# Kernel tuning notes

Measured on AMD Instinct MI355X. Metric: run time of the kernel, lower is better.

## Reference

```python
import jax, jax.numpy as jnp
import numpy as np
from jax import lax

BN_EPS = 1e-5
LN_EPS = 1e-5
EPS = 1e-6


def _bn(x, g, b, m, v):
    inv = g / jnp.sqrt(v + BN_EPS)
    return (x - m[None, :, None, None]) * inv[None, :, None, None] + b[None, :, None, None]


def _conv1x1(x, w, b=None):
    y = jnp.einsum('bchw,oc->bohw', x, w)
    if b is not None:
        y = y + b[None, :, None, None]
    return y


def _conv2d(x, w, pad_h, pad_w):
    return lax.conv_general_dilated(x, w, (1, 1), [(pad_h, pad_h), (pad_w, pad_w)],
                                    dimension_numbers=('NCHW', 'OIHW', 'NCHW'))


def _haar_dwt(x):
    # Haar analysis, stride-2: pure 2x2 add/sub arithmetic (H, W assumed even).
    B, C, H, W = x.shape
    xb = x.reshape(B, C, H // 2, 2, W // 2, 2)
    x00 = xb[:, :, :, 0, :, 0]; x01 = xb[:, :, :, 0, :, 1]
    x10 = xb[:, :, :, 1, :, 0]; x11 = xb[:, :, :, 1, :, 1]
    LL = 0.5 * (x00 + x01 + x10 + x11)
    LH = 0.5 * (-x00 + x01 - x10 + x11)
    HL = 0.5 * (-x00 - x01 + x10 + x11)
    HH = 0.5 * (x00 - x01 - x10 + x11)
    return LH, HL, HH, LL


def _haar_idwt(LH, HL, HH, LL):
    # Matches conv_transpose2d(stride=2) with the same Haar kernels.
    x00 = 0.5 * (LL - LH - HL + HH); x01 = 0.5 * (LL + LH - HL - HH)
    x10 = 0.5 * (LL - LH + HL - HH); x11 = 0.5 * (LL + LH + HL + HH)
    B, C, h, w = LL.shape
    top = jnp.stack([x00, x01], axis=-1)  # (B,C,h,w,2)
    bot = jnp.stack([x10, x11], axis=-1)
    y = jnp.stack([top, bot], axis=3)     # (B,C,h,2,w,2)
    return y.reshape(B, C, 2 * h, 2 * w)


def _soft_threshold(x, thr):
    return jnp.sign(x) * jax.nn.relu(jnp.abs(x) - thr)


def _forward(x, red_w, red_bias, red_bn_g, red_bn_b, red_bn_m, red_bn_v,
             gct_fc1_w, gct_fc1_b, gct_ln_g, gct_ln_b, gct_fc2_w, gct_fc2_b,
             rel_h_w, rel_h_b, rel_h_bn_g, rel_h_bn_b, rel_h_bn_m, rel_h_bn_v,
             rel_v_w, rel_v_b, rel_v_bn_g, rel_v_bn_b, rel_v_bn_m, rel_v_bn_v,
             rel_fus_w, rel_fus_b, hw_theta, hw_fuse_w, hw_fc_w, hw_fc_b,
             sf_w, sf_b, sf_bn_g, sf_bn_b, sf_bn_m, sf_bn_v, fin_w, fin_b):
    B, C, H, W = x.shape
    split = C // 2  # alpha = 0.5
    identity = x[:, :split]
    gate = x[:, split:]
    r = jax.nn.relu(_bn(_conv1x1(gate, red_w, red_bias), red_bn_g, red_bn_b, red_bn_m, red_bn_v))
    # --- GCT stream: GAP -> Linear -> LayerNorm -> ReLU -> Linear -> sigmoid gate ---
    ctx = r.mean(axis=(2, 3))                      # (B,Cr)
    h1 = ctx @ gct_fc1_w.T + gct_fc1_b
    mu = h1.mean(-1, keepdims=True)
    var = ((h1 - mu) ** 2).mean(-1, keepdims=True)
    h1 = (h1 - mu) / jnp.sqrt(var + LN_EPS) * gct_ln_g + gct_ln_b
    w_gct = jax.nn.sigmoid(jax.nn.relu(h1) @ gct_fc2_w.T + gct_fc2_b)
    gct_out = r * w_gct[:, :, None, None]
    # --- Rel stream: anisotropic pool -> conv/BN/ReLU -> bilinear(size-1 axis == broadcast) ---
    hf = _conv2d(r.mean(axis=2, keepdims=True), rel_h_w, 0, 1) + rel_h_b[None, :, None, None]
    hf = jax.nn.relu(_bn(hf, rel_h_bn_g, rel_h_bn_b, rel_h_bn_m, rel_h_bn_v))
    hf = jnp.broadcast_to(hf, (B, hf.shape[1], H, W))
    vf = _conv2d(r.mean(axis=3, keepdims=True), rel_v_w, 1, 0) + rel_v_b[None, :, None, None]
    vf = jax.nn.relu(_bn(vf, rel_v_bn_g, rel_v_bn_b, rel_v_bn_m, rel_v_bn_v))
    vf = jnp.broadcast_to(vf, (B, vf.shape[1], H, W))
    rel_w_map = jax.nn.sigmoid(_conv1x1(jnp.concatenate([hf, vf], axis=1), rel_fus_w, rel_fus_b))
    rel_out = r * rel_w_map
    # --- HWFE / wavelet attention ---
    LH, HL, HH, LL = _haar_dwt(r)
    t = jax.nn.sigmoid(hw_theta)                   # (3,Cr,1,1)
    m_LH = jnp.abs(LH).mean(axis=(2, 3), keepdims=True) + EPS
    m_HL = jnp.abs(HL).mean(axis=(2, 3), keepdims=True) + EPS
    m_HH = jnp.abs(HH).mean(axis=(2, 3), keepdims=True) + EPS
    LH_h = _soft_threshold(LH, t[0][None] * m_LH)
    HL_h = _soft_threshold(HL, t[1][None] * m_HL)
    HH_h = _soft_threshold(HH, t[2][None] * m_HH)
    fused = _conv1x1(jnp.concatenate([LH_h, HL_h, HH_h], axis=1), hw_fuse_w)
    X_re = _haar_idwt(LH_h, HL_h, fused, LL)       # note: fused sits in HH slot, as in source
    gap = X_re.mean(axis=(2, 3)) @ hw_fc_w.T + hw_fc_b
    attn = jax.nn.softmax(gap, axis=1)
    hwfe_out = r * attn[:, :, None, None]
    # --- stream fusion + gating ---
    interaction = gct_out * rel_out + hwfe_out
    gate_weight = jax.nn.sigmoid(_bn(_conv1x1(interaction, sf_w, sf_b), sf_bn_g, sf_bn_b, sf_bn_m, sf_bn_v))
    out = jnp.concatenate([identity, gate * gate_weight], axis=1)
    return _conv1x1(out, fin_w, fin_b)


def setup_inputs() -> dict:
    key = jax.random.key(0)
    ks = jax.random.split(key, 20)
    B, C, H, W = 16, 512, 64, 64
    Cg = C // 2           # gate channels = 256
    Cr = 16               # max(4, 256 // 16)
    Ch = Cr // 2          # 8
    Hd = max(1, Cr // 4)  # 4
    f = lambda k, s: jax.random.normal(k, s, jnp.float32) * 0.05
    return dict(
        x=jax.random.normal(ks[0], (B, C, H, W), jnp.float32),
        red_w=f(ks[1], (Cr, Cg)), red_bias=f(ks[2], (Cr,)),
        red_bn_g=jnp.ones((Cr,)), red_bn_b=jnp.zeros((Cr,)),
        red_bn_m=jnp.zeros((Cr,)), red_bn_v=jnp.ones((Cr,)),
        gct_fc1_w=f(ks[3], (Hd, Cr)), gct_fc1_b=f(ks[4], (Hd,)),
        gct_ln_g=jnp.ones((Hd,)), gct_ln_b=jnp.zeros((Hd,)),
        gct_fc2_w=f(ks[5], (Cr, Hd)), gct_fc2_b=f(ks[6], (Cr,)),
        rel_h_w=f(ks[7], (Ch, Cr, 1, 3)), rel_h_b=f(ks[8], (Ch,)),
        rel_h_bn_g=jnp.ones((Ch,)), rel_h_bn_b=jnp.zeros((Ch,)),
        rel_h_bn_m=jnp.zeros((Ch,)), rel_h_bn_v=jnp.ones((Ch,)),
        rel_v_w=f(ks[9], (Ch, Cr, 3, 1)), rel_v_b=f(ks[10], (Ch,)),
        rel_v_bn_g=jnp.ones((Ch,)), rel_v_bn_b=jnp.zeros((Ch,)),
        rel_v_bn_m=jnp.zeros((Ch,)), rel_v_bn_v=jnp.ones((Ch,)),
        rel_fus_w=f(ks[11], (Cr, 2 * Ch)), rel_fus_b=f(ks[12], (Cr,)),
        hw_theta=f(ks[13], (3, Cr, 1, 1)), hw_fuse_w=f(ks[14], (Cr, 3 * Cr)),
        hw_fc_w=f(ks[15], (Cr, Cr)), hw_fc_b=f(ks[16], (Cr,)),
        sf_w=f(ks[17], (Cg, Cr)), sf_b=f(ks[18], (Cg,)),
        sf_bn_g=jnp.ones((Cg,)), sf_bn_b=jnp.zeros((Cg,)),
        sf_bn_m=jnp.zeros((Cg,)), sf_bn_v=jnp.ones((Cg,)),
        fin_w=f(ks[19], (C, C)), fin_b=jnp.zeros((C,)),
    )


def reference(x, red_w, red_bias, red_bn_g, red_bn_b, red_bn_m, red_bn_v,
              gct_fc1_w, gct_fc1_b, gct_ln_g, gct_ln_b, gct_fc2_w, gct_fc2_b,
              rel_h_w, rel_h_b, rel_h_bn_g, rel_h_bn_b, rel_h_bn_m, rel_h_bn_v,
              rel_v_w, rel_v_b, rel_v_bn_g, rel_v_bn_b, rel_v_bn_m, rel_v_bn_v,
              rel_fus_w, rel_fus_b, hw_theta, hw_fuse_w, hw_fc_w, hw_fc_b,
              sf_w, sf_b, sf_bn_g, sf_bn_b, sf_bn_m, sf_bn_v, fin_w, fin_b):
    return _forward(x, red_w, red_bias, red_bn_g, red_bn_b, red_bn_m, red_bn_v,
                    gct_fc1_w, gct_fc1_b, gct_ln_g, gct_ln_b, gct_fc2_w, gct_fc2_b,
                    rel_h_w, rel_h_b, rel_h_bn_g, rel_h_bn_b, rel_h_bn_m, rel_h_bn_v,
                    rel_v_w, rel_v_b, rel_v_bn_g, rel_v_bn_b, rel_v_bn_m, rel_v_bn_v,
                    rel_fus_w, rel_fus_b, hw_theta, hw_fuse_w, hw_fc_w, hw_fc_b,
                    sf_w, sf_b, sf_bn_g, sf_bn_b, sf_bn_m, sf_bn_v, fin_w, fin_b)
```

## Files before the change

### kernel.cpp

```cpp
#include <hip/hip_runtime.h>
#include <cstdint>

typedef uint16_t u16;
typedef uint32_t u32;
typedef uint64_t u64;
typedef __attribute__((ext_vector_type(4))) float f32x4;
typedef __attribute__((ext_vector_type(8))) short bf16x8;

__device__ __forceinline__ u16 f2bf(float f) {
  union { float f; u32 i; } u; u.f = f;
  u32 r = u.i + 0x7FFFu + ((u.i >> 16) & 1u);
  return (u16)(r >> 16);
}
__device__ __forceinline__ float sigm(float x) { return 1.f / (1.f + __expf(-x)); }

__global__ __launch_bounds__(256) void k0_pack(
    const float* __restrict__ fw, u16* __restrict__ fwb)
{
  int i = blockIdx.x * 256 + threadIdx.x;
  f32x4 v = ((const f32x4*)fw)[i];
  u64 p = (u64)f2bf(v[0]) | ((u64)f2bf(v[1]) << 16) |
          ((u64)f2bf(v[2]) << 32) | ((u64)f2bf(v[3]) << 48);
  ((u64*)fwb)[i] = p;
}

__global__ __launch_bounds__(256) void k1_reduce(
    const float* __restrict__ x, const float* __restrict__ rw, const float* __restrict__ rb,
    const float* __restrict__ bg, const float* __restrict__ bb, const float* __restrict__ bm,
    const float* __restrict__ bv, float* __restrict__ r)
{
  __shared__ __align__(16) float wl[256][16];
  __shared__ float bl[16];
  __shared__ float sl[16];
  int t = threadIdx.x;
  if (t < 16) {
    float s = bg[t] * rsqrtf(bv[t] + 1e-5f);
    sl[t] = s;
    bl[t] = (rb[t] - bm[t]) * s + bb[t];
  }
  __syncthreads();
  for (int i = 0; i < 16; ++i) {
    int flat = i * 256 + t;
    int co = flat >> 8, c = flat & 255;
    wl[c][co] = rw[co * 256 + c] * sl[co];
  }
  __syncthreads();
  int p = blockIdx.x * 256 + t;
  int b = p >> 12, pp = p & 4095;
  const float* gsrc = x + ((size_t)(b * 512 + 256)) * 4096 + pp;
  float acc[16];
#pragma unroll
  for (int co = 0; co < 16; ++co) acc[co] = bl[co];
#pragma unroll 4
  for (int c = 0; c < 256; ++c) {
    float g = gsrc[(size_t)c * 4096];
    const f32x4* wr = (const f32x4*)(&wl[c][0]);
    f32x4 a0 = wr[0], a1 = wr[1], a2 = wr[2], a3 = wr[3];
    acc[0]  += g * a0[0]; acc[1]  += g * a0[1]; acc[2]  += g * a0[2]; acc[3]  += g * a0[3];
    acc[4]  += g * a1[0]; acc[5]  += g * a1[1]; acc[6]  += g * a1[2]; acc[7]  += g * a1[3];
    acc[8]  += g * a2[0]; acc[9]  += g * a2[1]; acc[10] += g * a2[2]; acc[11] += g * a2[3];
    acc[12] += g * a3[0]; acc[13] += g * a3[1]; acc[14] += g * a3[2]; acc[15] += g * a3[3];
  }
  float* rd = r + ((size_t)b * 16) * 4096 + pp;
#pragma unroll
  for (int co = 0; co < 16; ++co) rd[(size_t)co * 4096] = fmaxf(acc[co], 0.f);
}

__global__ __launch_bounds__(256) void k2_means(
    const float* __restrict__ r, float* __restrict__ cm, float* __restrict__ rm,
    float* __restrict__ ctx)
{
  __shared__ __align__(16) float tile[64][68];
  int bc = blockIdx.x, t = threadIdx.x;
  const float* src = r + (size_t)bc * 4096;
#pragma unroll
  for (int i = 0; i < 4; ++i) {
    int off = (i * 256 + t) * 4;
    int row = off >> 6, col = off & 63;
    f32x4 v = *(const f32x4*)(src + off);
    *(f32x4*)&tile[row][col] = v;
  }
  __syncthreads();
  int wv = t >> 6, lane = t & 63;
  if (wv == 0) {
    float s = 0.f;
    for (int h = 0; h < 64; ++h) s += tile[h][lane];
    cm[bc * 64 + lane] = s * (1.f / 64.f);
    float tot = s;
#pragma unroll
    for (int m = 32; m; m >>= 1) tot += __shfl_xor(tot, m, 64);
    if (lane == 0) ctx[bc] = tot * (1.f / 4096.f);
  } else if (wv == 1) {
    float s = 0.f;
    for (int w0 = 0; w0 < 64; ++w0) s += tile[lane][(w0 + lane) & 63];
    rm[bc * 64 + lane] = s * (1.f / 64.f);
  }
}

__global__ __launch_bounds__(256) void k3a_gct(
    const float* __restrict__ ctx,
    const float* f1w, const float* f1b, const float* lng, const float* lnb,
    const float* f2w, const float* f2b, const float* fcw, const float* fcb,
    float* __restrict__ wgct, float* __restrict__ attn)
{
  __shared__ float cl[256];
  __shared__ float gl[256];
  int t = threadIdx.x;
  cl[t] = ctx[t];
  __syncthreads();
  int b = t >> 4, c = t & 15;
  const float* cb = &cl[b * 16];
  float a[4];
#pragma unroll
  for (int j = 0; j < 4; ++j) {
    float s = f1b[j];
    for (int i = 0; i < 16; ++i) s += cb[i] * f1w[j * 16 + i];
    a[j] = s;
  }
  float mu = 0.25f * (a[0] + a[1] + a[2] + a[3]);
  float var = 0.f;
#pragma unroll
  for (int j = 0; j < 4; ++j) { float d = a[j] - mu; var += d * d; }
  var *= 0.25f;
  float inv = rsqrtf(var + 1e-5f);
#pragma unroll
  for (int j = 0; j < 4; ++j)
    a[j] = fmaxf((a[j] - mu) * inv * lng[j] + lnb[j], 0.f);
  float s2 = f2b[c];
#pragma unroll
  for (int j = 0; j < 4; ++j) s2 += a[j] * f2w[c * 4 + j];
  wgct[t] = sigm(s2);
  float g = fcb[c];
  for (int i = 0; i < 16; ++i) g += cb[i] * fcw[c * 16 + i];
  gl[t] = g;
  __syncthreads();
  const float* gb = &gl[b * 16];
  float mx = -1e30f;
  for (int i = 0; i < 16; ++i) mx = fmaxf(mx, gb[i]);
  float den = 0.f;
  for (int i = 0; i < 16; ++i) den += __expf(gb[i] - mx);
  attn[t] = __expf(g - mx) / den;
}

__global__ __launch_bounds__(64) void k3b_rel(
    const float* __restrict__ cm, const float* __restrict__ rm,
    const float* hw, const float* hb, const float* hbg, const float* hbb, const float* hbm, const float* hbv,
    const float* vw, const float* vb_, const float* vbg, const float* vbb, const float* vbm, const float* vbv,
    const float* fw, const float* fb, float* __restrict__ hfc, float* __restrict__ vfc)
{
  __shared__ float cml[16][64], rml[16][64];
  int b = blockIdx.x, t = threadIdx.x;
  for (int i = 0; i < 16; ++i) {
    cml[i][t] = cm[(b * 16 + i) * 64 + t];
    rml[i][t] = rm[(b * 16 + i) * 64 + t];
  }
  __syncthreads();
  float hf[8], vf[8];
  for (int o = 0; o < 8; ++o) {
    float sh = 0.f, sv = 0.f;
    for (int ci = 0; ci < 16; ++ci) {
#pragma unroll
      for (int kk = 0; kk < 3; ++kk) {
        int q = t + kk - 1;
        bool ok = (q >= 0 && q < 64);
        int qi = ok ? q : 0;
        float xh = ok ? cml[ci][qi] : 0.f;
        float xv = ok ? rml[ci][qi] : 0.f;
        sh += hw[(o * 16 + ci) * 3 + kk] * xh;
        sv += vw[(o * 16 + ci) * 3 + kk] * xv;
      }
    }
    float s1 = hbg[o] * rsqrtf(hbv[o] + 1e-5f);
    hf[o] = fmaxf((sh + hb[o] - hbm[o]) * s1 + hbb[o], 0.f);
    float s2 = vbg[o] * rsqrtf(vbv[o] + 1e-5f);
    vf[o] = fmaxf((sv + vb_[o] - vbm[o]) * s2 + vbb[o], 0.f);
  }
  for (int o = 0; o < 16; ++o) {
    float sh = fb[o], sv = 0.f;
#pragma unroll
    for (int c = 0; c < 8; ++c) {
      sh += fw[o * 16 + c] * hf[c];
      sv += fw[o * 16 + 8 + c] * vf[c];
    }
    hfc[(b * 16 + o) * 64 + t] = sh;
    vfc[(b * 16 + o) * 64 + t] = sv;
  }
}

__global__ __launch_bounds__(512, 4) void k45_v2(
    const float* __restrict__ x, const float* __restrict__ r,
    const float* __restrict__ wgct, const float* __restrict__ attn,
    const float* __restrict__ hfc, const float* __restrict__ vfc,
    const float* __restrict__ sfw, const float* __restrict__ sfb,
    const float* __restrict__ sg, const float* __restrict__ sb_,
    const float* __restrict__ sbm, const float* __restrict__ sbv,
    const u16* __restrict__ fwb, const float* __restrict__ fb,
    float* __restrict__ out)
{
  __shared__ __align__(16) u16 A[64 * 528];
  __shared__ float wgs[16], ats[16], vfhs[16];
  char* Ab = (char*)A;

  int bid = blockIdx.x;
  int b = bid >> 6, h = bid & 63;
  int t = threadIdx.x;

  if (t < 16) {
    wgs[t]  = wgct[b * 16 + t];
    ats[t]  = attn[b * 16 + t];
    vfhs[t] = vfc[(b * 16 + t) * 64 + h];
  }
  if (t < 256) {
    int o = t;
    float s = sg[o] * rsqrtf(sbv[o] + 1e-5f);
    float* wrow = (float*)(Ab + (o & 63) * 1056 + 512 + (o >> 6) * 64);
#pragma unroll
    for (int k2 = 0; k2 < 16; ++k2) wrow[k2] = sfw[o * 16 + k2] * s;
    *(float*)(Ab + (o & 63) * 1056 + 768 + (o >> 6) * 4) =
        (sfb[o] - sbm[o]) * s + sb_[o];
  }
  __syncthreads();

#pragma unroll
  for (int i = 0; i < 2; ++i) {
    int idx = i * 512 + t;
    int k = idx >> 6, w = idx & 63;
    float rv = r[((size_t)(b * 16 + k)) * 4096 + h * 64 + w];
    float rel = sigm(hfc[(b * 16 + k) * 64 + w] + vfhs[k]);
    *(float*)(Ab + w * 1056 + 784 + k * 4) =
        rv * rv * wgs[k] * rel + rv * ats[k];
  }
  __syncthreads();

  {
    int w = t & 63, og = t >> 6;
    float iv[16];
#pragma unroll
    for (int k2 = 0; k2 < 16; ++k2)
      iv[k2] = *(const float*)(Ab + w * 1056 + 784 + k2 * 4);
    const float* gsrc = x + ((size_t)(b * 512 + 256)) * 4096 + h * 64 + w;
    for (int j = 0; j < 32; ++j) {
      int o = og * 32 + j;
      const f32x4* wr = (const f32x4*)(Ab + (o & 63) * 1056 + 512 + (o >> 6) * 64);
      f32x4 w0 = wr[0], w1 = wr[1], w2 = wr[2], w3 = wr[3];
      float dot = *(const float*)(Ab + (o & 63) * 1056 + 768 + (o >> 6) * 4);
      dot += iv[0]  * w0[0] + iv[1]  * w0[1] + iv[2]  * w0[2] + iv[3]  * w0[3];
      dot += iv[4]  * w1[0] + iv[5]  * w1[1] + iv[6]  * w1[2] + iv[7]  * w1[3];
      dot += iv[8]  * w2[0] + iv[9]  * w2[1] + iv[10] * w2[2] + iv[11] * w2[3];
      dot += iv[12] * w3[0] + iv[13] * w3[1] + iv[14] * w3[2] + iv[15] * w3[3];
      float gwv = sigm(dot);
      float gv = gsrc[(size_t)o * 4096];
      A[w * 528 + o] = f2bf(gv * gwv);
    }
  }
  __syncthreads();

#pragma unroll
  for (int i = 0; i < 8; ++i) {
    int flat = i * 512 + t;
    int c = flat >> 4, q = flat & 15;
    f32x4 v = *(const f32x4*)(x + ((size_t)(b * 512 + c)) * 4096 + h * 64 + q * 4);
#pragma unroll
    for (int j = 0; j < 4; ++j) A[(q * 4 + j) * 528 + 256 + c] = f2bf(v[j]);
  }
  __syncthreads();

  int lane = t & 63, wv = t >> 6;
  int fr = lane & 15, quad = lane >> 4;
  int n0w = wv * 64;
  f32x4 acc[4][4];
#pragma unroll
  for (int j = 0; j < 4; ++j) {
    float bvv = fb[n0w + j * 16 + fr];
    f32x4 b4 = {bvv, bvv, bvv, bvv};
#pragma unroll
    for (int i = 0; i < 4; ++i) acc[i][j] = b4;
  }
  const u16* Bp = fwb + (size_t)(n0w + fr) * 512 + quad * 8;
  for (int kb = 0; kb < 16; ++kb) {
    int c0 = kb * 32 + quad * 8;
    int kbb = kb ^ 8;
    bf16x8 af[4], bfr[4];
#pragma unroll
    for (int i = 0; i < 4; ++i)
      af[i] = *(const bf16x8*)(A + (i * 16 + fr) * 528 + c0);
#pragma unroll
    for (int j = 0; j < 4; ++j)
      bfr[j] = *(const bf16x8*)(Bp + (size_t)(j * 16) * 512 + kbb * 32);
#pragma unroll
    for (int j = 0; j < 4; ++j)
#pragma unroll
      for (int i = 0; i < 4; ++i)
        acc[i][j] = __builtin_amdgcn_mfma_f32_16x16x32_bf16(af[i], bfr[j], acc[i][j], 0, 0, 0);
  }

  float* ob = out + ((size_t)(b * 512 + n0w + fr)) * 4096 + h * 64 + quad * 4;
#pragma unroll
  for (int j = 0; j < 4; ++j)
#pragma unroll
    for (int i = 0; i < 4; ++i)
      *(f32x4*)(ob + (size_t)(j * 16) * 4096 + i * 16) = acc[i][j];
}

extern "C" void kernel_launch(void* const* d_in, const int* in_sizes, int n_in,
                              void* d_out, int out_size, void* d_ws, size_t ws_size,
                              hipStream_t stream) {
  const float* x      = (const float*)d_in[0];
  const float* red_w  = (const float*)d_in[1];
  const float* red_b  = (const float*)d_in[2];
  const float* rbg    = (const float*)d_in[3];
  const float* rbb    = (const float*)d_in[4];
  const float* rbm    = (const float*)d_in[5];
  const float* rbv    = (const float*)d_in[6];
  const float* f1w    = (const float*)d_in[7];
  const float* f1b    = (const float*)d_in[8];
  const float* lng    = (const float*)d_in[9];
  const float* lnb    = (const float*)d_in[10];
  const float* f2w    = (const float*)d_in[11];
  const float* f2b    = (const float*)d_in[12];
  const float* rhw    = (const float*)d_in[13];
  const float* rhb    = (const float*)d_in[14];
  const float* rhbg   = (const float*)d_in[15];
  const float* rhbb   = (const float*)d_in[16];
  const float* rhbm   = (const float*)d_in[17];
  const float* rhbv   = (const float*)d_in[18];
  const float* rvw    = (const float*)d_in[19];
  const float* rvb    = (const float*)d_in[20];
  const float* rvbg   = (const float*)d_in[21];
  const float* rvbb   = (const float*)d_in[22];
  const float* rvbm   = (const float*)d_in[23];
  const float* rvbv   = (const float*)d_in[24];
  const float* fusw   = (const float*)d_in[25];
  const float* fusb   = (const float*)d_in[26];
  const float* fcw    = (const float*)d_in[29];
  const float* fcb    = (const float*)d_in[30];
  const float* sfw    = (const float*)d_in[31];
  const float* sfb    = (const float*)d_in[32];
  const float* sbg    = (const float*)d_in[33];
  const float* sbb    = (const float*)d_in[34];
  const float* sbm    = (const float*)d_in[35];
  const float* sbv    = (const float*)d_in[36];
  const float* finw   = (const float*)d_in[37];
  const float* finb   = (const float*)d_in[38];
  float* out = (float*)d_out;

  char* ws = (char*)d_ws;
  size_t off = 0;
  float* r   = (float*)(ws + off); off += (size_t)16 * 16 * 4096 * 4;
  u16*   fwb = (u16*)(ws + off);   off += (size_t)512 * 512 * 2;
  float* cm  = (float*)(ws + off); off += 65536;
  float* rm  = (float*)(ws + off); off += 65536;
  float* ctx = (float*)(ws + off); off += 1024;
  float* wg  = (float*)(ws + off); off += 1024;
  float* at  = (float*)(ws + off); off += 1024;
  float* hfc = (float*)(ws + off); off += 65536;
  float* vfc = (float*)(ws + off); off += 65536;

  k0_pack<<<256, 256, 0, stream>>>(finw, fwb);
  k1_reduce<<<256, 256, 0, stream>>>(x, red_w, red_b, rbg, rbb, rbm, rbv, r);
  k2_means<<<256, 256, 0, stream>>>(r, cm, rm, ctx);
  k3a_gct<<<1, 256, 0, stream>>>(ctx, f1w, f1b, lng, lnb, f2w, f2b, fcw, fcb, wg, at);
  k3b_rel<<<16, 64, 0, stream>>>(cm, rm, rhw, rhb, rhbg, rhbb, rhbm, rhbv,
                                 rvw, rvb, rvbg, rvbb, rvbm, rvbv, fusw, fusb, hfc, vfc);
  k45_v2<<<1024, 512, 0, stream>>>(x, r, wg, at, hfc, vfc,
                                   sfw, sfb, sbg, sbb, sbm, sbv, fwb, finb, out);
}
```

Baseline: 440.4 us.

## Merge small prologue kernels into one launch and vectorize LDS staging in main kernel

The weight-pack, GCT and relation kernels become one launch, with the block index choosing the branch, so two launches and their serialization gaps go away. The main kernel removes one barrier, shrinks the LDS row stride, and writes the gated tile as 8-wide bf16 vectors instead of scalar u16 stores. The identity-channel transpose now uses ds_bpermute lane shuffles so each lane packs four bf16 values into a single 64-bit LDS store. The reduce loop unroll also goes from 4 to 8. These changes add shuffle instructions and rely on the new stride giving acceptable LDS bank behaviour.

```diff
diff --git a/kernel.cpp b/kernel.cpp
--- a/kernel.cpp
+++ b/kernel.cpp
@@ -13,16 +13,6 @@
   return (u16)(r >> 16);
 }
 __device__ __forceinline__ float sigm(float x) { return 1.f / (1.f + __expf(-x)); }
-
-__global__ __launch_bounds__(256) void k0_pack(
-    const float* __restrict__ fw, u16* __restrict__ fwb)
-{
-  int i = blockIdx.x * 256 + threadIdx.x;
-  f32x4 v = ((const f32x4*)fw)[i];
-  u64 p = (u64)f2bf(v[0]) | ((u64)f2bf(v[1]) << 16) |
-          ((u64)f2bf(v[2]) << 32) | ((u64)f2bf(v[3]) << 48);
-  ((u64*)fwb)[i] = p;
-}
 
 __global__ __launch_bounds__(256) void k1_reduce(
     const float* __restrict__ x, const float* __restrict__ rw, const float* __restrict__ rb,
@@ -51,7 +41,7 @@
   float acc[16];
 #pragma unroll
   for (int co = 0; co < 16; ++co) acc[co] = bl[co];
-#pragma unroll 4
+#pragma unroll 8
   for (int c = 0; c < 256; ++c) {
     float g = gsrc[(size_t)c * 4096];
     const f32x4* wr = (const f32x4*)(&wl[c][0]);
@@ -97,97 +87,108 @@
   }
 }
 
-__global__ __launch_bounds__(256) void k3a_gct(
+__global__ __launch_bounds__(256) void k3x(
+    const float* __restrict__ finw, u16* __restrict__ fwb,
     const float* __restrict__ ctx,
     const float* f1w, const float* f1b, const float* lng, const float* lnb,
     const float* f2w, const float* f2b, const float* fcw, const float* fcb,
-    float* __restrict__ wgct, float* __restrict__ attn)
-{
-  __shared__ float cl[256];
-  __shared__ float gl[256];
-  int t = threadIdx.x;
-  cl[t] = ctx[t];
-  __syncthreads();
-  int b = t >> 4, c = t & 15;
-  const float* cb = &cl[b * 16];
-  float a[4];
-#pragma unroll
-  for (int j = 0; j < 4; ++j) {
-    float s = f1b[j];
-    for (int i = 0; i < 16; ++i) s += cb[i] * f1w[j * 16 + i];
-    a[j] = s;
-  }
-  float mu = 0.25f * (a[0] + a[1] + a[2] + a[3]);
-  float var = 0.f;
-#pragma unroll
-  for (int j = 0; j < 4; ++j) { float d = a[j] - mu; var += d * d; }
-  var *= 0.25f;
-  float inv = rsqrtf(var + 1e-5f);
-#pragma unroll
-  for (int j = 0; j < 4; ++j)
-    a[j] = fmaxf((a[j] - mu) * inv * lng[j] + lnb[j], 0.f);
-  float s2 = f2b[c];
-#pragma unroll
-  for (int j = 0; j < 4; ++j) s2 += a[j] * f2w[c * 4 + j];
-  wgct[t] = sigm(s2);
-  float g = fcb[c];
-  for (int i = 0; i < 16; ++i) g += cb[i] * fcw[c * 16 + i];
-  gl[t] = g;
-  __syncthreads();
-  const float* gb = &gl[b * 16];
-  float mx = -1e30f;
-  for (int i = 0; i < 16; ++i) mx = fmaxf(mx, gb[i]);
-  float den = 0.f;
-  for (int i = 0; i < 16; ++i) den += __expf(gb[i] - mx);
-  attn[t] = __expf(g - mx) / den;
-}
-
-__global__ __launch_bounds__(64) void k3b_rel(
+    float* __restrict__ wgct, float* __restrict__ attn,
     const float* __restrict__ cm, const float* __restrict__ rm,
     const float* hw, const float* hb, const float* hbg, const float* hbb, const float* hbm, const float* hbv,
     const float* vw, const float* vb_, const float* vbg, const float* vbb, const float* vbm, const float* vbv,
     const float* fw, const float* fb, float* __restrict__ hfc, float* __restrict__ vfc)
 {
-  __shared__ float cml[16][64], rml[16][64];
-  int b = blockIdx.x, t = threadIdx.x;
-  for (int i = 0; i < 16; ++i) {
-    cml[i][t] = cm[(b * 16 + i) * 64 + t];
-    rml[i][t] = rm[(b * 16 + i) * 64 + t];
-  }
-  __syncthreads();
-  float hf[8], vf[8];
-  for (int o = 0; o < 8; ++o) {
-    float sh = 0.f, sv = 0.f;
-    for (int ci = 0; ci < 16; ++ci) {
-#pragma unroll
-      for (int kk = 0; kk < 3; ++kk) {
-        int q = t + kk - 1;
-        bool ok = (q >= 0 && q < 64);
-        int qi = ok ? q : 0;
-        float xh = ok ? cml[ci][qi] : 0.f;
-        float xv = ok ? rml[ci][qi] : 0.f;
-        sh += hw[(o * 16 + ci) * 3 + kk] * xh;
-        sv += vw[(o * 16 + ci) * 3 + kk] * xv;
+  int bid = blockIdx.x, t = threadIdx.x;
+  if (bid < 256) {
+    int i = bid * 256 + t;
+    f32x4 v = ((const f32x4*)finw)[i];
+    u64 p = (u64)f2bf(v[0]) | ((u64)f2bf(v[1]) << 16) |
+            ((u64)f2bf(v[2]) << 32) | ((u64)f2bf(v[3]) << 48);
+    ((u64*)fwb)[i] = p;
+  } else if (bid == 256) {
+    __shared__ float cl[256];
+    __shared__ float gl[256];
+    cl[t] = ctx[t];
+    __syncthreads();
+    int b = t >> 4, c = t & 15;
+    const float* cb = &cl[b * 16];
+    float a[4];
+#pragma unroll
+    for (int j = 0; j < 4; ++j) {
+      float s = f1b[j];
+      for (int i = 0; i < 16; ++i) s += cb[i] * f1w[j * 16 + i];
+      a[j] = s;
+    }
+    float mu = 0.25f * (a[0] + a[1] + a[2] + a[3]);
+    float var = 0.f;
+#pragma unroll
+    for (int j = 0; j < 4; ++j) { float d = a[j] - mu; var += d * d; }
+    var *= 0.25f;
+    float inv = rsqrtf(var + 1e-5f);
+#pragma unroll
+    for (int j = 0; j < 4; ++j)
+      a[j] = fmaxf((a[j] - mu) * inv * lng[j] + lnb[j], 0.f);
+    float s2 = f2b[c];
+#pragma unroll
+    for (int j = 0; j < 4; ++j) s2 += a[j] * f2w[c * 4 + j];
+    wgct[t] = sigm(s2);
+    float g = fcb[c];
+    for (int i = 0; i < 16; ++i) g += cb[i] * fcw[c * 16 + i];
+    gl[t] = g;
+    __syncthreads();
+    const float* gb = &gl[b * 16];
+    float mx = -1e30f;
+    for (int i = 0; i < 16; ++i) mx = fmaxf(mx, gb[i]);
+    float den = 0.f;
+    for (int i = 0; i < 16; ++i) den += __expf(gb[i] - mx);
+    attn[t] = __expf(g - mx) / den;
+  } else {
+    __shared__ float cml[16][64], rml[16][64];
+    int b = bid - 257;
+#pragma unroll
+    for (int i = 0; i < 4; ++i) {
+      int idx = i * 256 + t;
+      int row = idx >> 6, col = idx & 63;
+      cml[row][col] = cm[(b * 16 + row) * 64 + col];
+      rml[row][col] = rm[(b * 16 + row) * 64 + col];
+    }
+    __syncthreads();
+    if (t < 64) {
+      float hf[8], vf[8];
+      for (int o = 0; o < 8; ++o) {
+        float sh = 0.f, sv = 0.f;
+        for (int ci = 0; ci < 16; ++ci) {
+#pragma unroll
+          for (int kk = 0; kk < 3; ++kk) {
+            int q = t + kk - 1;
+            bool ok = (q >= 0 && q < 64);
+            int qi = ok ? q : 0;
+            float xh = ok ? cml[ci][qi] : 0.f;
+            float xv = ok ? rml[ci][qi] : 0.f;
+            sh += hw[(o * 16 + ci) * 3 + kk] * xh;
+            sv += vw[(o * 16 + ci) * 3 + kk] * xv;
+          }
+        }
+        float s1 = hbg[o] * rsqrtf(hbv[o] + 1e-5f);
+        hf[o] = fmaxf((sh + hb[o] - hbm[o]) * s1 + hbb[o], 0.f);
+        float s2 = vbg[o] * rsqrtf(vbv[o] + 1e-5f);
+        vf[o] = fmaxf((sv + vb_[o] - vbm[o]) * s2 + vbb[o], 0.f);
       }
-    }
-    float s1 = hbg[o] * rsqrtf(hbv[o] + 1e-5f);
-    hf[o] = fmaxf((sh + hb[o] - hbm[o]) * s1 + hbb[o], 0.f);
-    float s2 = vbg[o] * rsqrtf(vbv[o] + 1e-5f);
-    vf[o] = fmaxf((sv + vb_[o] - vbm[o]) * s2 + vbb[o], 0.f);
-  }
-  for (int o = 0; o < 16; ++o) {
-    float sh = fb[o], sv = 0.f;
-#pragma unroll
-    for (int c = 0; c < 8; ++c) {
-      sh += fw[o * 16 + c] * hf[c];
-      sv += fw[o * 16 + 8 + c] * vf[c];
-    }
-    hfc[(b * 16 + o) * 64 + t] = sh;
-    vfc[(b * 16 + o) * 64 + t] = sv;
-  }
-}
-
-__global__ __launch_bounds__(512, 4) void k45_v2(
+      for (int o = 0; o < 16; ++o) {
+        float sh = fb[o], sv = 0.f;
+#pragma unroll
+        for (int c = 0; c < 8; ++c) {
+          sh += fw[o * 16 + c] * hf[c];
+          sv += fw[o * 16 + 8 + c] * vf[c];
+        }
+        hfc[(b * 16 + o) * 64 + t] = sh;
+        vfc[(b * 16 + o) * 64 + t] = sv;
+      }
+    }
+  }
+}
+
+__global__ __launch_bounds__(512, 4) void k45_v3(
     const float* __restrict__ x, const float* __restrict__ r,
     const float* __restrict__ wgct, const float* __restrict__ attn,
     const float* __restrict__ hfc, const float* __restrict__ vfc,
@@ -197,75 +198,91 @@
     const u16* __restrict__ fwb, const float* __restrict__ fb,
     float* __restrict__ out)
 {
-  __shared__ __align__(16) u16 A[64 * 528];
-  __shared__ float wgs[16], ats[16], vfhs[16];
+  __shared__ __align__(16) u16 A[64 * 520];
   char* Ab = (char*)A;
 
   int bid = blockIdx.x;
   int b = bid >> 6, h = bid & 63;
   int t = threadIdx.x;
-
-  if (t < 16) {
-    wgs[t]  = wgct[b * 16 + t];
-    ats[t]  = attn[b * 16 + t];
-    vfhs[t] = vfc[(b * 16 + t) * 64 + h];
-  }
+  int lane = t & 63, wv = t >> 6;
+
   if (t < 256) {
     int o = t;
     float s = sg[o] * rsqrtf(sbv[o] + 1e-5f);
-    float* wrow = (float*)(Ab + (o & 63) * 1056 + 512 + (o >> 6) * 64);
-#pragma unroll
-    for (int k2 = 0; k2 < 16; ++k2) wrow[k2] = sfw[o * 16 + k2] * s;
-    *(float*)(Ab + (o & 63) * 1056 + 768 + (o >> 6) * 4) =
+    const f32x4* sw = (const f32x4*)(sfw + o * 16);
+    f32x4 w0 = sw[0] * s, w1 = sw[1] * s, w2 = sw[2] * s, w3 = sw[3] * s;
+    f32x4* wrow = (f32x4*)(Ab + (o & 63) * 1040 + 512 + (o >> 6) * 64);
+    wrow[0] = w0; wrow[1] = w1; wrow[2] = w2; wrow[3] = w3;
+    *(float*)(Ab + (o & 63) * 1040 + 768 + (o >> 6) * 4) =
         (sfb[o] - sbm[o]) * s + sb_[o];
   }
-  __syncthreads();
-
 #pragma unroll
   for (int i = 0; i < 2; ++i) {
     int idx = i * 512 + t;
     int k = idx >> 6, w = idx & 63;
     float rv = r[((size_t)(b * 16 + k)) * 4096 + h * 64 + w];
-    float rel = sigm(hfc[(b * 16 + k) * 64 + w] + vfhs[k]);
-    *(float*)(Ab + w * 1056 + 784 + k * 4) =
-        rv * rv * wgs[k] * rel + rv * ats[k];
+    float rel = sigm(hfc[(b * 16 + k) * 64 + w] + vfc[(b * 16 + k) * 64 + h]);
+    *(float*)(Ab + w * 1040 + 784 + k * 4) =
+        rv * rv * wgct[b * 16 + k] * rel + rv * attn[b * 16 + k];
   }
   __syncthreads();
 
   {
     int w = t & 63, og = t >> 6;
-    float iv[16];
-#pragma unroll
-    for (int k2 = 0; k2 < 16; ++k2)
-      iv[k2] = *(const float*)(Ab + w * 1056 + 784 + k2 * 4);
+    const char* irow = Ab + w * 1040 + 784;
+    f32x4 iv0 = *(const f32x4*)(irow);
+    f32x4 iv1 = *(const f32x4*)(irow + 16);
+    f32x4 iv2 = *(const f32x4*)(irow + 32);
+    f32x4 iv3 = *(const f32x4*)(irow + 48);
     const float* gsrc = x + ((size_t)(b * 512 + 256)) * 4096 + h * 64 + w;
-    for (int j = 0; j < 32; ++j) {
-      int o = og * 32 + j;
-      const f32x4* wr = (const f32x4*)(Ab + (o & 63) * 1056 + 512 + (o >> 6) * 64);
-      f32x4 w0 = wr[0], w1 = wr[1], w2 = wr[2], w3 = wr[3];
-      float dot = *(const float*)(Ab + (o & 63) * 1056 + 768 + (o >> 6) * 4);
-      dot += iv[0]  * w0[0] + iv[1]  * w0[1] + iv[2]  * w0[2] + iv[3]  * w0[3];
-      dot += iv[4]  * w1[0] + iv[5]  * w1[1] + iv[6]  * w1[2] + iv[7]  * w1[3];
-      dot += iv[8]  * w2[0] + iv[9]  * w2[1] + iv[10] * w2[2] + iv[11] * w2[3];
-      dot += iv[12] * w3[0] + iv[13] * w3[1] + iv[14] * w3[2] + iv[15] * w3[3];
-      float gwv = sigm(dot);
-      float gv = gsrc[(size_t)o * 4096];
-      A[w * 528 + o] = f2bf(gv * gwv);
-    }
-  }
-  __syncthreads();
-
-#pragma unroll
-  for (int i = 0; i < 8; ++i) {
-    int flat = i * 512 + t;
-    int c = flat >> 4, q = flat & 15;
-    f32x4 v = *(const f32x4*)(x + ((size_t)(b * 512 + c)) * 4096 + h * 64 + q * 4);
-#pragma unroll
-    for (int j = 0; j < 4; ++j) A[(q * 4 + j) * 528 + 256 + c] = f2bf(v[j]);
-  }
-  __syncthreads();
-
-  int lane = t & 63, wv = t >> 6;
+#pragma unroll
+    for (int jo = 0; jo < 4; ++jo) {
+      bf16x8 vb;
+#pragma unroll
+      for (int jj = 0; jj < 8; ++jj) {
+        int o = og * 32 + jo * 8 + jj;
+        const char* orow = Ab + (o & 63) * 1040;
+        const f32x4* wr = (const f32x4*)(orow + 512 + (o >> 6) * 64);
+        f32x4 w0 = wr[0], w1 = wr[1], w2 = wr[2], w3 = wr[3];
+        float dot = *(const float*)(orow + 768 + (o >> 6) * 4);
+        dot += iv0[0] * w0[0] + iv0[1] * w0[1] + iv0[2] * w0[2] + iv0[3] * w0[3];
+        dot += iv1[0] * w1[0] + iv1[1] * w1[1] + iv1[2] * w1[2] + iv1[3] * w1[3];
+        dot += iv2[0] * w2[0] + iv2[1] * w2[1] + iv2[2] * w2[2] + iv2[3] * w2[3];
+        dot += iv3[0] * w3[0] + iv3[1] * w3[1] + iv3[2] * w3[2] + iv3[3] * w3[3];
+        float gwv = sigm(dot);
+        float gv = gsrc[(size_t)o * 4096];
+        vb[jj] = (short)f2bf(gv * gwv);
+      }
+      *(bf16x8*)(Ab + w * 1040 + (og * 32 + jo * 8) * 2) = vb;
+    }
+  }
+  __syncthreads();
+
+  {
+    int q = lane & 15, cg = lane >> 4;
+    int qp = lane & 15, jp = lane >> 4;
+    int m = qp * 4 + jp;
+#pragma unroll
+    for (int i = 0; i < 8; ++i) {
+      int c = i * 32 + wv * 4 + cg;
+      f32x4 v = *(const f32x4*)(x + ((size_t)(b * 512 + c)) * 4096 + h * 64 + q * 4);
+      u32 w01 = (u32)f2bf(v[0]) | ((u32)f2bf(v[1]) << 16);
+      u32 w23 = (u32)f2bf(v[2]) | ((u32)f2bf(v[3]) << 16);
+      u32 e[4];
+#pragma unroll
+      for (int cp = 0; cp < 4; ++cp) {
+        int srcaddr = (cp * 16 + qp) << 2;
+        u32 r01 = (u32)__builtin_amdgcn_ds_bpermute(srcaddr, (int)w01);
+        u32 r23 = (u32)__builtin_amdgcn_ds_bpermute(srcaddr, (int)w23);
+        u32 sel = (jp < 2) ? r01 : r23;
+        e[cp] = (jp & 1) ? (sel >> 16) : (sel & 0xffffu);
+      }
+      u64 pk = (u64)e[0] | ((u64)e[1] << 16) | ((u64)e[2] << 32) | ((u64)e[3] << 48);
+      *(u64*)(Ab + m * 1040 + 512 + (i * 32 + wv * 4) * 2) = pk;
+    }
+  }
+  __syncthreads();
+
   int fr = lane & 15, quad = lane >> 4;
   int n0w = wv * 64;
   f32x4 acc[4][4];
@@ -283,7 +300,7 @@
     bf16x8 af[4], bfr[4];
 #pragma unroll
     for (int i = 0; i < 4; ++i)
-      af[i] = *(const bf16x8*)(A + (i * 16 + fr) * 528 + c0);
+      af[i] = *(const bf16x8*)(A + (i * 16 + fr) * 520 + c0);
 #pragma unroll
     for (int j = 0; j < 4; ++j)
       bfr[j] = *(const bf16x8*)(Bp + (size_t)(j * 16) * 512 + kbb * 32);
@@ -356,12 +373,12 @@
   float* hfc = (float*)(ws + off); off += 65536;
   float* vfc = (float*)(ws + off); off += 65536;
 
-  k0_pack<<<256, 256, 0, stream>>>(finw, fwb);
   k1_reduce<<<256, 256, 0, stream>>>(x, red_w, red_b, rbg, rbb, rbm, rbv, r);
   k2_means<<<256, 256, 0, stream>>>(r, cm, rm, ctx);
-  k3a_gct<<<1, 256, 0, stream>>>(ctx, f1w, f1b, lng, lnb, f2w, f2b, fcw, fcb, wg, at);
-  k3b_rel<<<16, 64, 0, stream>>>(cm, rm, rhw, rhb, rhbg, rhbb, rhbm, rhbv,
-                                 rvw, rvb, rvbg, rvbb, rvbm, rvbv, fusw, fusb, hfc, vfc);
-  k45_v2<<<1024, 512, 0, stream>>>(x, r, wg, at, hfc, vfc,
+  k3x<<<273, 256, 0, stream>>>(finw, fwb,
+                               ctx, f1w, f1b, lng, lnb, f2w, f2b, fcw, fcb, wg, at,
+                               cm, rm, rhw, rhb, rhbg, rhbb, rhbm, rhbv,
+                               rvw, rvb, rvbg, rvbb, rvbm, rvbv, fusw, fusb, hfc, vfc);
+  k45_v3<<<1024, 512, 0, stream>>>(x, r, wg, at, hfc, vfc,
                                    sfw, sfb, sbg, sbb, sbm, sbv, fwb, finb, out);
 }
```

Result: faster. 423.5 us (-3.8%).
